# Kernel optimization log

Measured on AMD Instinct MI355X. Metric: run time of the kernel, lower is better.

## Reference

```python
import jax, jax.numpy as jnp
import numpy as np

B, S, D, H, FF, R = 4, 1024, 1024, 16, 4096, 128
DH = D // H


def rmsnorm(x, w, eps=1e-6):
    # matches torch: norm = ||x||_2 / sqrt(d); out = w * x / (norm + eps)
    n = jnp.sqrt(jnp.sum(x * x, axis=-1, keepdims=True)) / np.sqrt(x.shape[-1]).astype(np.float32)
    return w * x / (n + eps)


def setup_inputs() -> dict:
    key = jax.random.key(0)
    ks = jax.random.split(key, 20)
    def w(k, shape, s=0.02):
        return (jax.random.normal(k, shape, jnp.float32) * s)
    return {
        "x": jax.random.normal(ks[0], (B, S, D), jnp.float32),
        "norm1_w": jnp.ones((D,), jnp.float32),
        "Wq": w(ks[1], (D, D)), "bq": jnp.zeros((D,), jnp.float32),
        "Wk": w(ks[2], (D, D)), "bk": jnp.zeros((D,), jnp.float32),
        "Wv": w(ks[3], (D, D)), "bv": jnp.zeros((D,), jnp.float32),
        "Wz": w(ks[4], (D, D)), "bz": jnp.zeros((D,), jnp.float32),
        "Wg": w(ks[5], (D, D)), "bg": jnp.zeros((D,), jnp.float32),
        "gdw": w(ks[6], (R, D)), "gdb": jnp.zeros((R,), jnp.float32),
        "guw": w(ks[7], (D, R)), "gub": jnp.zeros((D,), jnp.float32),
        "Wo": w(ks[8], (D, D)), "bo": jnp.zeros((D,), jnp.float32),
        "norm2_w": jnp.ones((D,), jnp.float32),
        "f1w": w(ks[9], (FF, D)), "f1b": jnp.zeros((FF,), jnp.float32),
        "f2w": w(ks[10], (D, FF)), "f2b": jnp.zeros((D,), jnp.float32),
    }


def reference(x, norm1_w, Wq, bq, Wk, bk, Wv, bv, Wz, bz, Wg, bg,
              gdw, gdb, guw, gub, Wo, bo, norm2_w, f1w, f1b, f2w, f2b):
    b, s, d = x.shape
    h = d // DH
    # 1. Norm + Q/K/V/Z projections
    xn = rmsnorm(x, norm1_w)
    q = xn @ Wq.T + bq
    k = xn @ Wk.T + bk
    v = xn @ Wv.T + bv
    z = xn @ Wz.T + bz
    # 2-3. DPG decay: gamma_t = clamp(sigmoid(W_up ReLU(W_down z_t)))
    gamma = jax.nn.sigmoid(jax.nn.relu(z @ gdw.T + gdb) @ guw.T + gub)
    gamma = jnp.clip(gamma, 1e-6, 1.0 - 1e-6)
    # 4. Core recurrence: h_t = z_t * sigmoid(W_g h_{t-1}) + gamma_t * h_{t-1}
    def step(hprev, zg):
        zt, gt = zg
        hn = zt * jax.nn.sigmoid(hprev @ Wg.T + bg) + gt * hprev
        return hn, hn
    h0 = jnp.zeros((b, d), x.dtype)
    _, hs = jax.lax.scan(step, h0, (jnp.swapaxes(z, 0, 1), jnp.swapaxes(gamma, 0, 1)))
    hseq = jnp.swapaxes(hs, 0, 1)  # [B,S,D]
    # 5. Multi-head attention over Q,K,V
    qh = q.reshape(b, s, h, DH)
    kh = k.reshape(b, s, h, DH)
    vh = v.reshape(b, s, h, DH)
    scores = jnp.einsum('bqhd,bkhd->bhqk', qh, kh) / np.sqrt(DH).astype(np.float32)
    attn = jax.nn.softmax(scores, axis=-1)
    ao = jnp.einsum('bhqk,bkhd->bqhd', attn, vh).reshape(b, s, d)
    ao = ao @ Wo.T + bo
    # 6. Residuals
    y = x + ao + hseq
    # 7. FFN + output
    yn = rmsnorm(y, norm2_w)
    ff = jax.nn.gelu(yn @ f1w.T + f1b) @ f2w.T + f2b
    return y + ff
```

## Files before the change

kernel.cpp:

```cpp
#include <hip/hip_runtime.h>
#include <stdint.h>

#define DD 1024
#define SS 1024
#define NBS 32

typedef __attribute__((ext_vector_type(8))) __bf16 bf16x8;
typedef __attribute__((ext_vector_type(4))) float f32x4;

union Frag { uint4 u; bf16x8 b; };

__device__ __forceinline__ float bf2f(ushort u){ union{uint32_t i; float f;} c; c.i = ((uint32_t)u)<<16; return c.f; }
__device__ __forceinline__ float bflo(uint32_t p){ union{uint32_t i; float f;} c; c.i = p<<16; return c.f; }
__device__ __forceinline__ float bfhi(uint32_t p){ union{uint32_t i; float f;} c; c.i = p & 0xffff0000u; return c.f; }
__device__ __forceinline__ ushort f2bf(float f){
  union{float f; uint32_t u;} c; c.f = f;
  uint32_t u = c.u;
  return (ushort)((u + 0x7fffu + ((u>>16)&1u)) >> 16);
}

__global__ __launch_bounds__(256) void cast_k(const float* __restrict__ s,
    ushort* __restrict__ d, int n)
{
  int i = (blockIdx.x*256 + threadIdx.x)*4;
  if (i >= n) return;
  float4 v = *(const float4*)(s+i);
  ushort4 o; o.x=f2bf(v.x); o.y=f2bf(v.y); o.z=f2bf(v.z); o.w=f2bf(v.w);
  *(ushort4*)(d+i) = o;
}

__global__ __launch_bounds__(256) void rmsnorm_k(const float* __restrict__ X,
    const float* __restrict__ w, ushort* __restrict__ out)
{
  const int row = blockIdx.x, t = threadIdx.x;
  const float* x = X + (size_t)row*DD;
  float xs[4]; float s = 0.f;
  #pragma unroll
  for (int i=0;i<4;i++){ float v = x[t + i*256]; xs[i]=v; s += v*v; }
  #pragma unroll
  for (int off=32; off>0; off>>=1) s += __shfl_xor(s, off, 64);
  __shared__ float sred[4];
  if ((t&63)==0) sred[t>>6] = s;
  __syncthreads();
  s = sred[0]+sred[1]+sred[2]+sred[3];
  float inv = 1.f/(sqrtf(s)*0.03125f + 1e-6f);
  #pragma unroll
  for (int i=0;i<4;i++){
    int c2 = t + i*256;
    out[(size_t)row*DD + c2] = f2bf(xs[i]*inv*w[c2]);
  }
}

enum { ACT_NONE=0, ACT_RELU=1, ACT_SIG=2, ACT_GELU=3 };
enum { EPI_B16=0, EPI_DUAL=1, EPI_F32=2, EPI_Y=3, EPI_OUT=4 };

template<int ACT, int EPI>
__global__ __launch_bounds__(256) void gemm_bt(
    const ushort* __restrict__ A, const ushort* __restrict__ W,
    const float* __restrict__ bias, int N, int K,
    ushort* __restrict__ Ob, float* __restrict__ Of,
    const float* __restrict__ X32, const ushort* __restrict__ H16,
    const float* __restrict__ Yf)
{
  __shared__ __align__(16) ushort At[128*32];
  __shared__ __align__(16) ushort Wt[128*32];
  const int tid = threadIdx.x;
  const int wave = tid >> 6, lane = tid & 63;
  const int quad = lane >> 4, l16 = lane & 15;
  const int wr = wave >> 1, wc = wave & 1;
  const int m0 = blockIdx.x * 128, n0 = blockIdx.y * 128;

  f32x4 acc[4][4];
  const f32x4 vz = {0.f,0.f,0.f,0.f};
  #pragma unroll
  for (int i=0;i<4;i++)
    #pragma unroll
    for (int j=0;j<4;j++) acc[i][j] = vz;

  const ushort* gA = A + (size_t)(m0 + wave*32 + (lane>>2))*K + (lane&3)*8;
  const ushort* gW = W + (size_t)(n0 + wave*32 + (lane>>2))*K + (lane&3)*8;
  ushort* lA = At + wave*1024 + lane*8;
  ushort* lW = Wt + wave*1024 + lane*8;

  for (int ko = 0; ko < K; ko += 32) {
    uint4 va  = *(const uint4*)(gA + ko);
    uint4 va2 = *(const uint4*)(gA + ko + (size_t)16*K);
    uint4 vw  = *(const uint4*)(gW + ko);
    uint4 vw2 = *(const uint4*)(gW + ko + (size_t)16*K);
    __syncthreads();
    *(uint4*)lA          = va;
    *(uint4*)(lA + 512)  = va2;
    *(uint4*)lW          = vw;
    *(uint4*)(lW + 512)  = vw2;
    __syncthreads();
    Frag af[4], bfr[4];
    #pragma unroll
    for (int mi=0;mi<4;mi++)
      af[mi].u = *(const uint4*)&At[(wr*64 + mi*16 + l16)*32 + quad*8];
    #pragma unroll
    for (int ni=0;ni<4;ni++)
      bfr[ni].u = *(const uint4*)&Wt[(wc*64 + ni*16 + l16)*32 + quad*8];
    #pragma unroll
    for (int mi=0;mi<4;mi++)
      #pragma unroll
      for (int ni=0;ni<4;ni++)
        acc[mi][ni] = __builtin_amdgcn_mfma_f32_16x16x32_bf16(af[mi].b, bfr[ni].b, acc[mi][ni], 0,0,0);
  }

  float bia[4];
  #pragma unroll
  for (int ni=0;ni<4;ni++) bia[ni] = bias[n0 + wc*64 + ni*16 + l16];
  #pragma unroll
  for (int mi=0;mi<4;mi++) {
    const int row0 = m0 + wr*64 + mi*16 + quad*4;
    #pragma unroll
    for (int ni=0;ni<4;ni++) {
      const int col = n0 + wc*64 + ni*16 + l16;
      #pragma unroll
      for (int r=0;r<4;r++) {
        float vx = acc[mi][ni][r] + bia[ni];
        if (ACT == ACT_RELU) vx = fmaxf(vx, 0.f);
        else if (ACT == ACT_SIG) {
          vx = 1.f/(1.f+__expf(-vx));
          vx = fminf(fmaxf(vx, 1e-6f), 1.f-1e-6f);
        } else if (ACT == ACT_GELU) {
          float ci = 0.7978845608028654f*(vx + 0.044715f*vx*vx*vx);
          float th = 1.f - 2.f/(1.f + __expf(2.f*ci));
          vx = 0.5f*vx*(1.f+th);
        }
        size_t idx = (size_t)(row0 + r)*N + col;
        if (EPI == EPI_B16)      Ob[idx] = f2bf(vx);
        else if (EPI == EPI_DUAL){ Ob[idx] = f2bf(vx); Of[idx] = vx; }
        else if (EPI == EPI_F32)  Of[idx] = vx;
        else if (EPI == EPI_Y)    Of[idx] = vx + X32[idx] + bf2f(H16[idx]);
        else                      Of[idx] = vx + Yf[idx];
      }
    }
  }
}

__global__ __launch_bounds__(256) void attn_k(const ushort* __restrict__ q,
  const ushort* __restrict__ k, const ushort* __restrict__ v, ushort* __restrict__ ao)
{
  __shared__ __align__(16) ushort Ks[64*64];
  __shared__ __align__(16) ushort Vs[64*64];
  __shared__ float Ps[64*65];
  const int qt = blockIdx.x, bh = blockIdx.y;
  const int b = bh >> 4, h = bh & 15;
  const int t = threadIdx.x, r = t >> 2, seg = t & 3;
  const ushort* qrow = q + ((size_t)(b*SS + qt*64 + r))*DD + h*64;
  float qr[64];
  #pragma unroll
  for (int i=0;i<64;i+=8){
    uint4 u = *(const uint4*)(qrow + i);
    qr[i+0]=bflo(u.x); qr[i+1]=bfhi(u.x); qr[i+2]=bflo(u.y); qr[i+3]=bfhi(u.y);
    qr[i+4]=bflo(u.z); qr[i+5]=bfhi(u.z); qr[i+6]=bflo(u.w); qr[i+7]=bfhi(u.w);
  }
  float o[16];
  #pragma unroll
  for (int i=0;i<16;i++) o[i]=0.f;
  float mrun = -1e30f, lrun = 0.f;
  const int jrow = t >> 3, jch = t & 7;
  for (int kt=0; kt<16; kt++) {
    __syncthreads();
    const ushort* kg = k + ((size_t)(b*SS + kt*64))*DD + h*64;
    const ushort* vg = v + ((size_t)(b*SS + kt*64))*DD + h*64;
    #pragma unroll
    for (int part=0; part<2; part++){
      int j = jrow + part*32;
      *(uint4*)&Ks[j*64 + jch*8] = *(const uint4*)(kg + (size_t)j*DD + jch*8);
      *(uint4*)&Vs[j*64 + jch*8] = *(const uint4*)(vg + (size_t)j*DD + jch*8);
    }
    __syncthreads();
    float sc[16];
    #pragma unroll
    for (int jj=0;jj<16;jj++){
      int j = seg*16 + jj;
      float s_ = 0.f;
      #pragma unroll
      for (int i=0;i<64;i+=8){
        uint4 u = *(const uint4*)&Ks[j*64+i];
        s_ = fmaf(qr[i+0], bflo(u.x), s_); s_ = fmaf(qr[i+1], bfhi(u.x), s_);
        s_ = fmaf(qr[i+2], bflo(u.y), s_); s_ = fmaf(qr[i+3], bfhi(u.y), s_);
        s_ = fmaf(qr[i+4], bflo(u.z), s_); s_ = fmaf(qr[i+5], bfhi(u.z), s_);
        s_ = fmaf(qr[i+6], bflo(u.w), s_); s_ = fmaf(qr[i+7], bfhi(u.w), s_);
      }
      sc[jj] = s_ * 0.125f;
    }
    float mx = sc[0];
    #pragma unroll
    for (int jj=1;jj<16;jj++) mx = fmaxf(mx, sc[jj]);
    mx = fmaxf(mx, __shfl_xor(mx, 1, 64));
    mx = fmaxf(mx, __shfl_xor(mx, 2, 64));
    float mnew = fmaxf(mrun, mx);
    float psum = 0.f;
    #pragma unroll
    for (int jj=0;jj<16;jj++){
      float p = __expf(sc[jj]-mnew);
      Ps[r*65 + seg*16 + jj] = p;
      psum += p;
    }
    psum += __shfl_xor(psum, 1, 64);
    psum += __shfl_xor(psum, 2, 64);
    float alpha = __expf(mrun - mnew);
    lrun = lrun*alpha + psum;
    mrun = mnew;
    #pragma unroll
    for (int i=0;i<16;i++) o[i] *= alpha;
    __syncthreads();
    #pragma unroll 4
    for (int j=0;j<64;j++){
      float pj = Ps[r*65 + j];
      uint4 u0 = *(const uint4*)&Vs[j*64 + seg*16];
      uint4 u1 = *(const uint4*)&Vs[j*64 + seg*16 + 8];
      o[ 0]=fmaf(pj,bflo(u0.x),o[ 0]); o[ 1]=fmaf(pj,bfhi(u0.x),o[ 1]);
      o[ 2]=fmaf(pj,bflo(u0.y),o[ 2]); o[ 3]=fmaf(pj,bfhi(u0.y),o[ 3]);
      o[ 4]=fmaf(pj,bflo(u0.z),o[ 4]); o[ 5]=fmaf(pj,bfhi(u0.z),o[ 5]);
      o[ 6]=fmaf(pj,bflo(u0.w),o[ 6]); o[ 7]=fmaf(pj,bfhi(u0.w),o[ 7]);
      o[ 8]=fmaf(pj,bflo(u1.x),o[ 8]); o[ 9]=fmaf(pj,bfhi(u1.x),o[ 9]);
      o[10]=fmaf(pj,bflo(u1.y),o[10]); o[11]=fmaf(pj,bfhi(u1.y),o[11]);
      o[12]=fmaf(pj,bflo(u1.z),o[12]); o[13]=fmaf(pj,bfhi(u1.z),o[13]);
      o[14]=fmaf(pj,bflo(u1.w),o[14]); o[15]=fmaf(pj,bfhi(u1.w),o[15]);
    }
  }
  float invl = 1.f/lrun;
  ushort* orow = ao + ((size_t)(b*SS + qt*64 + r))*DD + h*64 + seg*16;
  #pragma unroll
  for (int i=0;i<16;i++) orow[i] = f2bf(o[i]*invl);
}

__global__ __launch_bounds__(256) void scan_k(
    const ushort* __restrict__ Wgb, const float* __restrict__ bg,
    const float* __restrict__ z32, const float* __restrict__ gm32,
    ushort* __restrict__ hseq, ushort* __restrict__ hstate)
{
  const int blk = blockIdx.x, t = threadIdx.x;
  const int wave = t>>6, lane = t&63, quad = lane>>4, c = lane&15;
  const int mt = wave & 1, kh = wave >> 1;
  const int nbase = blk*32 + mt*16;
  const bool epi = (kh == 0) && (c < 4);
  const int n0w = nbase + quad*4;
  Frag a[16];
  {
    const ushort* wrow = Wgb + (size_t)(nbase + c)*DD + kh*512 + quad*8;
    #pragma unroll
    for (int kt=0;kt<16;kt++) a[kt].u = *(const uint4*)(wrow + kt*32);
  }
  float bgv[4];
  #pragma unroll
  for (int r=0;r<4;r++) bgv[r] = bg[nbase + quad*4 + r];
  __shared__ __align__(16) ushort Hs[2][4096];
  __shared__ float redbuf[2][64][5];
  const int qi = (c*1024 + n0w) >> 2;
  int gmax = 256;

  float4 znx = {0,0,0,0}, gnx = {0,0,0,0};
  if (epi) {
    znx = *(const float4*)(z32  + ((size_t)c*SS + 0)*DD + n0w);
    gnx = *(const float4*)(gm32 + ((size_t)c*SS + 0)*DD + n0w);
  }

  for (int st=0; st<SS; st++) {
    const int cur = st & 1;
    if (st > 0) {
      const char* hrd = (const char*)(hstate + ((st+3)&3)*4096) + t*32;
      uint4 va, vb;
      int guard = 0;
      for (;;) {
        __builtin_amdgcn_fence(__ATOMIC_ACQUIRE, "agent");
        asm volatile(
          "global_load_dwordx4 %0, %2, off\n\t"
          "global_load_dwordx4 %1, %2, off offset:16\n\t"
          "s_waitcnt vmcnt(0)"
          : "=&v"(va), "=&v"(vb) : "v"(hrd) : "memory");
        bool ok = (va.x!=0xFFFFFFFFu)&(va.y!=0xFFFFFFFFu)
                & (va.z!=0xFFFFFFFFu)&(va.w!=0xFFFFFFFFu)
                & (vb.x!=0xFFFFFFFFu)&(vb.y!=0xFFFFFFFFu)
                & (vb.z!=0xFFFFFFFFu)&(vb.w!=0xFFFFFFFFu);
        if (ok) break;
        if (++guard > gmax) { gmax = 0; break; }
        if (guard > 3) __builtin_amdgcn_s_sleep(1);
      }
      if (epi) {
        uint64_t* rst = (uint64_t*)(hstate + ((st+2)&3)*4096);
        __hip_atomic_store(rst + qi, 0xFFFFFFFFFFFFFFFFull,
                           __ATOMIC_RELAXED, __HIP_MEMORY_SCOPE_AGENT);
      }
      uint4* hsd = (uint4*)Hs[cur];
      hsd[t*2  ] = va;
      hsd[t*2+1] = vb;
    }
    float4 zc = znx, gc = gnx;
    if (epi && (st+1 < SS)) {
      znx = *(const float4*)(z32  + ((size_t)c*SS + (st+1))*DD + n0w);
      gnx = *(const float4*)(gm32 + ((size_t)c*SS + (st+1))*DD + n0w);
    }
    if (st > 0) {
      asm volatile("s_waitcnt lgkmcnt(0)\ns_barrier" ::: "memory");
    }
    f32x4 acc = {0.f,0.f,0.f,0.f};
    if (st > 0) {
      f32x4 acc1 = {0.f,0.f,0.f,0.f};
      const uint4 z4 = make_uint4(0u,0u,0u,0u);
      #pragma unroll
      for (int kt=0;kt<16;kt+=2) {
        Frag b0, b1;
        b0.u = (c<4) ? *(const uint4*)&Hs[cur][c*1024 + kh*512 + (kt  )*32 + quad*8] : z4;
        b1.u = (c<4) ? *(const uint4*)&Hs[cur][c*1024 + kh*512 + (kt+1)*32 + quad*8] : z4;
        acc  = __builtin_amdgcn_mfma_f32_16x16x32_bf16(a[kt  ].b, b0.b, acc,  0,0,0);
        acc1 = __builtin_amdgcn_mfma_f32_16x16x32_bf16(a[kt+1].b, b1.b, acc1, 0,0,0);
      }
      #pragma unroll
      for (int r=0;r<4;r++) acc[r] += acc1[r];
    }
    if (kh == 1) {
      #pragma unroll
      for (int r=0;r<4;r++) redbuf[mt][lane][r] = acc[r];
    }
    asm volatile("s_waitcnt lgkmcnt(0)\ns_barrier" ::: "memory");
    if (epi) {
      ushort hb[4];
      float zr[4] = {zc.x, zc.y, zc.z, zc.w};
      float gr[4] = {gc.x, gc.y, gc.z, gc.w};
      #pragma unroll
      for (int r=0;r<4;r++) {
        float g = acc[r] + redbuf[mt][lane][r] + bgv[r];
        g = 1.f/(1.f+__expf(-g));
        float hp = (st>0) ? bf2f(Hs[cur][c*1024 + n0w + r]) : 0.f;
        hb[r] = f2bf(zr[r]*g + gr[r]*hp);
      }
      uint32_t p0 = (uint32_t)hb[0] | ((uint32_t)hb[1]<<16);
      uint32_t p1 = (uint32_t)hb[2] | ((uint32_t)hb[3]<<16);
      uint64_t pk = ((uint64_t)p1<<32) | (uint64_t)p0;
      uint64_t* hwd = (uint64_t*)(hstate + (st&3)*4096);
      __hip_atomic_store(hwd + qi, pk, __ATOMIC_RELAXED, __HIP_MEMORY_SCOPE_AGENT);
      uint2* sq = (uint2*)(hseq + ((size_t)c*SS + st)*DD + n0w);
      *sq = make_uint2(p0, p1);
    }
  }
}

extern "C" void kernel_launch(void* const* d_in, const int* in_sizes, int n_in,
                              void* d_out, int out_size, void* d_ws, size_t ws_size,
                              hipStream_t stream)
{
  const float* x   = (const float*)d_in[0];
  const float* n1w = (const float*)d_in[1];
  const float* Wq  = (const float*)d_in[2];
  const float* bq  = (const float*)d_in[3];
  const float* Wk  = (const float*)d_in[4];
  const float* bk  = (const float*)d_in[5];
  const float* Wv  = (const float*)d_in[6];
  const float* bv  = (const float*)d_in[7];
  const float* Wz  = (const float*)d_in[8];
  const float* bz  = (const float*)d_in[9];
  const float* Wg_ = (const float*)d_in[10];
  const float* bg  = (const float*)d_in[11];
  const float* gdw = (const float*)d_in[12];
  const float* gdb = (const float*)d_in[13];
  const float* guw = (const float*)d_in[14];
  const float* gub = (const float*)d_in[15];
  const float* Wo  = (const float*)d_in[16];
  const float* bo  = (const float*)d_in[17];
  const float* n2w = (const float*)d_in[18];
  const float* f1w = (const float*)d_in[19];
  const float* f1b = (const float*)d_in[20];
  const float* f2w = (const float*)d_in[21];
  const float* f2b = (const float*)d_in[22];

  char* ws = (char*)d_ws;
  const size_t MB = (size_t)1<<20;
  ushort* Wqb  = (ushort*)(ws +  0*MB);
  ushort* Wkb  = (ushort*)(ws +  2*MB);
  ushort* Wvb  = (ushort*)(ws +  4*MB);
  ushort* Wzb  = (ushort*)(ws +  6*MB);
  ushort* Wob  = (ushort*)(ws +  8*MB);
  ushort* Wgb  = (ushort*)(ws + 10*MB);
  ushort* gdwb = (ushort*)(ws + 12*MB);
  ushort* guwb = (ushort*)(ws + 12*MB + (512<<10));
  ushort* f1wb = (ushort*)(ws + 13*MB);
  ushort* f2wb = (ushort*)(ws + 21*MB);
  ushort* xn   = (ushort*)(ws + 29*MB);
  ushort* qb   = (ushort*)(ws + 37*MB);
  ushort* kb   = (ushort*)(ws + 45*MB);
  ushort* vb   = (ushort*)(ws + 53*MB);
  ushort* zb16 = (ushort*)(ws + 61*MB);
  ushort* ff1  = (ushort*)(ws + 37*MB);
  ushort* t1   = (ushort*)(ws + 69*MB);
  ushort* hseq = (ushort*)(ws + 70*MB);
  ushort* aob  = (ushort*)(ws + 78*MB);
  float*  zb32 = (float*) (ws + 86*MB);
  float*  yf   = (float*) (ws + 86*MB);
  float*  gm32 = (float*) (ws +102*MB);
  ushort* hst  = (ushort*)(ws +118*MB);
  ushort* yn = xn;

  cast_k<<<1024, 256, 0, stream>>>(Wq,  Wqb, 1048576);
  cast_k<<<1024, 256, 0, stream>>>(Wk,  Wkb, 1048576);
  cast_k<<<1024, 256, 0, stream>>>(Wv,  Wvb, 1048576);
  cast_k<<<1024, 256, 0, stream>>>(Wz,  Wzb, 1048576);
  cast_k<<<1024, 256, 0, stream>>>(Wo,  Wob, 1048576);
  cast_k<<<1024, 256, 0, stream>>>(Wg_, Wgb, 1048576);
  cast_k<<< 128, 256, 0, stream>>>(gdw, gdwb, 131072);
  cast_k<<< 128, 256, 0, stream>>>(guw, guwb, 131072);
  cast_k<<<4096, 256, 0, stream>>>(f1w, f1wb, 4194304);
  cast_k<<<4096, 256, 0, stream>>>(f2w, f2wb, 4194304);
  rmsnorm_k<<<4096, 256, 0, stream>>>(x, n1w, xn);
  gemm_bt<ACT_NONE,EPI_B16 ><<<dim3(32,8), 256, 0, stream>>>(xn, Wqb, bq, 1024, 1024, qb,  nullptr, nullptr, nullptr, nullptr);
  gemm_bt<ACT_NONE,EPI_B16 ><<<dim3(32,8), 256, 0, stream>>>(xn, Wkb, bk, 1024, 1024, kb,  nullptr, nullptr, nullptr, nullptr);
  gemm_bt<ACT_NONE,EPI_B16 ><<<dim3(32,8), 256, 0, stream>>>(xn, Wvb, bv, 1024, 1024, vb,  nullptr, nullptr, nullptr, nullptr);
  gemm_bt<ACT_NONE,EPI_DUAL><<<dim3(32,8), 256, 0, stream>>>(xn, Wzb, bz, 1024, 1024, zb16, zb32,   nullptr, nullptr, nullptr);
  gemm_bt<ACT_RELU,EPI_B16><<<dim3(32,1), 256, 0, stream>>>(zb16, gdwb, gdb, 128, 1024, t1, nullptr, nullptr, nullptr, nullptr);
  gemm_bt<ACT_SIG ,EPI_F32><<<dim3(32,8), 256, 0, stream>>>(t1, guwb, gub, 1024, 128, nullptr, gm32, nullptr, nullptr, nullptr);
  attn_k<<<dim3(16,64), 256, 0, stream>>>(qb, kb, vb, aob);
  (void)hipMemsetAsync(hst, 0xFF, 32768, stream);
  scan_k<<<dim3(NBS), 256, 0, stream>>>(Wgb, bg, zb32, gm32, hseq, hst);
  gemm_bt<ACT_NONE,EPI_Y><<<dim3(32,8), 256, 0, stream>>>(aob, Wob, bo, 1024, 1024, nullptr, yf, x, hseq, nullptr);
  rmsnorm_k<<<4096, 256, 0, stream>>>(yf, n2w, yn);
  gemm_bt<ACT_GELU,EPI_B16><<<dim3(32,32), 256, 0, stream>>>(yn, f1wb, f1b, 4096, 1024, ff1, nullptr, nullptr, nullptr, nullptr);
  gemm_bt<ACT_NONE,EPI_OUT><<<dim3(32,8), 256, 0, stream>>>(ff1, f2wb, f2b, 1024, 4096, nullptr, (float*)d_out, nullptr, nullptr, yf);
}
```

Before: 5.115 ms.

## Replace sentinel-polling handoff in scan with per-step atomic counter barrier

The recurrent scan's cross-block handoff changes. Before, each thread polled the shared h-state buffer for the absence of 0xFF sentinels and reset slots for a 4-deep ring. Now each block increments a per-step counter with release semantics, and waiters spin on one counter word before an acquire fence and a plain load from a double-buffered state. The goal is a cheaper spin loop, no sentinel reset stores, and less polling traffic. In exchange it adds an extra barrier at step 0, moves the z/gamma prefetch later in the loop, and relies on the fence ordering and a wider guard timeout being correct.

Result: slower. 9.432 ms (+84.4%).

```diff
diff --git a/kernel.cpp b/kernel.cpp
--- a/kernel.cpp
+++ b/kernel.cpp
@@ -232,7 +232,8 @@
 __global__ __launch_bounds__(256) void scan_k(
     const ushort* __restrict__ Wgb, const float* __restrict__ bg,
     const float* __restrict__ z32, const float* __restrict__ gm32,
-    ushort* __restrict__ hseq, ushort* __restrict__ hstate)
+    ushort* __restrict__ hseq, ushort* __restrict__ hstate,
+    uint32_t* __restrict__ cnt)
 {
   const int blk = blockIdx.x, t = threadIdx.x;
   const int wave = t>>6, lane = t&63, quad = lane>>4, c = lane&15;
@@ -252,7 +253,7 @@
   __shared__ __align__(16) ushort Hs[2][4096];
   __shared__ float redbuf[2][64][5];
   const int qi = (c*1024 + n0w) >> 2;
-  int gmax = 256;
+  int gmax = 4096;
 
   float4 znx = {0,0,0,0}, gnx = {0,0,0,0};
   if (epi) {
@@ -263,41 +264,25 @@
   for (int st=0; st<SS; st++) {
     const int cur = st & 1;
     if (st > 0) {
-      const char* hrd = (const char*)(hstate + ((st+3)&3)*4096) + t*32;
-      uint4 va, vb;
+      const uint32_t tgt = ((uint32_t)((st-1)>>3) + 1u) * 1024u;
+      const uint32_t* cp = cnt + ((st-1)&7)*16;
       int guard = 0;
       for (;;) {
-        __builtin_amdgcn_fence(__ATOMIC_ACQUIRE, "agent");
-        asm volatile(
-          "global_load_dwordx4 %0, %2, off\n\t"
-          "global_load_dwordx4 %1, %2, off offset:16\n\t"
-          "s_waitcnt vmcnt(0)"
-          : "=&v"(va), "=&v"(vb) : "v"(hrd) : "memory");
-        bool ok = (va.x!=0xFFFFFFFFu)&(va.y!=0xFFFFFFFFu)
-                & (va.z!=0xFFFFFFFFu)&(va.w!=0xFFFFFFFFu)
-                & (vb.x!=0xFFFFFFFFu)&(vb.y!=0xFFFFFFFFu)
-                & (vb.z!=0xFFFFFFFFu)&(vb.w!=0xFFFFFFFFu);
-        if (ok) break;
+        uint32_t v = __hip_atomic_load(cp, __ATOMIC_RELAXED, __HIP_MEMORY_SCOPE_AGENT);
+        if (v >= tgt) break;
         if (++guard > gmax) { gmax = 0; break; }
-        if (guard > 3) __builtin_amdgcn_s_sleep(1);
+        if (guard > 8) __builtin_amdgcn_s_sleep(1);
       }
-      if (epi) {
-        uint64_t* rst = (uint64_t*)(hstate + ((st+2)&3)*4096);
-        __hip_atomic_store(rst + qi, 0xFFFFFFFFFFFFFFFFull,
-                           __ATOMIC_RELAXED, __HIP_MEMORY_SCOPE_AGENT);
-      }
+      __builtin_amdgcn_fence(__ATOMIC_ACQUIRE, "agent");
+      const uint4* hrd = (const uint4*)((const char*)(hstate + ((st-1)&1)*4096) + (size_t)t*32);
+      uint4 va = hrd[0];
+      uint4 vb = hrd[1];
       uint4* hsd = (uint4*)Hs[cur];
       hsd[t*2  ] = va;
       hsd[t*2+1] = vb;
     }
     float4 zc = znx, gc = gnx;
-    if (epi && (st+1 < SS)) {
-      znx = *(const float4*)(z32  + ((size_t)c*SS + (st+1))*DD + n0w);
-      gnx = *(const float4*)(gm32 + ((size_t)c*SS + (st+1))*DD + n0w);
-    }
-    if (st > 0) {
-      asm volatile("s_waitcnt lgkmcnt(0)\ns_barrier" ::: "memory");
-    }
+    asm volatile("s_waitcnt lgkmcnt(0)\ns_barrier" ::: "memory");
     f32x4 acc = {0.f,0.f,0.f,0.f};
     if (st > 0) {
       f32x4 acc1 = {0.f,0.f,0.f,0.f};
@@ -332,10 +317,17 @@
       uint32_t p0 = (uint32_t)hb[0] | ((uint32_t)hb[1]<<16);
       uint32_t p1 = (uint32_t)hb[2] | ((uint32_t)hb[3]<<16);
       uint64_t pk = ((uint64_t)p1<<32) | (uint64_t)p0;
-      uint64_t* hwd = (uint64_t*)(hstate + (st&3)*4096);
+      uint64_t* hwd = (uint64_t*)(hstate + (st&1)*4096);
       __hip_atomic_store(hwd + qi, pk, __ATOMIC_RELAXED, __HIP_MEMORY_SCOPE_AGENT);
-      uint2* sq = (uint2*)(hseq + ((size_t)c*SS + st)*DD + n0w);
-      *sq = make_uint2(p0, p1);
+      uint64_t* sq = (uint64_t*)(hseq + ((size_t)c*SS + st)*DD + n0w);
+      __hip_atomic_store(sq, pk, __ATOMIC_RELAXED, __HIP_MEMORY_SCOPE_AGENT);
+    }
+    if (kh == 0 && lane == 0)
+      __hip_atomic_fetch_add(cnt + (st&7)*16, 16u,
+                             __ATOMIC_RELEASE, __HIP_MEMORY_SCOPE_AGENT);
+    if (epi && (st+1 < SS)) {
+      znx = *(const float4*)(z32  + ((size_t)c*SS + (st+1))*DD + n0w);
+      gnx = *(const float4*)(gm32 + ((size_t)c*SS + (st+1))*DD + n0w);
     }
   }
 }
@@ -393,6 +385,7 @@
   float*  yf   = (float*) (ws + 86*MB);
   float*  gm32 = (float*) (ws +102*MB);
   ushort* hst  = (ushort*)(ws +118*MB);
+  uint32_t* cnt = (uint32_t*)(ws +118*MB + (64<<10));
   ushort* yn = xn;
 
   cast_k<<<1024, 256, 0, stream>>>(Wq,  Wqb, 1048576);
@@ -413,8 +406,8 @@
   gemm_bt<ACT_RELU,EPI_B16><<<dim3(32,1), 256, 0, stream>>>(zb16, gdwb, gdb, 128, 1024, t1, nullptr, nullptr, nullptr, nullptr);
   gemm_bt<ACT_SIG ,EPI_F32><<<dim3(32,8), 256, 0, stream>>>(t1, guwb, gub, 1024, 128, nullptr, gm32, nullptr, nullptr, nullptr);
   attn_k<<<dim3(16,64), 256, 0, stream>>>(qb, kb, vb, aob);
-  (void)hipMemsetAsync(hst, 0xFF, 32768, stream);
-  scan_k<<<dim3(NBS), 256, 0, stream>>>(Wgb, bg, zb32, gm32, hseq, hst);
+  (void)hipMemsetAsync(cnt, 0, 512, stream);
+  scan_k<<<dim3(NBS), 256, 0, stream>>>(Wgb, bg, zb32, gm32, hseq, hst, cnt);
   gemm_bt<ACT_NONE,EPI_Y><<<dim3(32,8), 256, 0, stream>>>(aob, Wob, bo, 1024, 1024, nullptr, yf, x, hseq, nullptr);
   rmsnorm_k<<<4096, 256, 0, stream>>>(yf, n2w, yn);
   gemm_bt<ACT_GELU,EPI_B16><<<dim3(32,32), 256, 0, stream>>>(yn, f1wb, f1b, 4096, 1024, ff1, nullptr, nullptr, nullptr, nullptr);
```
